# Optimization experiments

Hardware: AMD Instinct MI355X
Metric: run time of the kernel (lower is better)

Reference implementation:

```python
import jax, jax.numpy as jnp
import numpy as np
from jax import lax

# ---- config (FalconH1Mixer, FalconH1-1.5B-like) ----
BATCH = 2
SEQ = 2048
HID = 2048
EXPAND = 2
INTER = EXPAND * HID          # 4096 (mamba_d_ssm=None)
HEADS = 64
PDIM = INTER // HEADS         # 64 head_dim
NSTATE = 128                  # mamba_d_state
G = 1                         # mamba_n_groups
HPG = HEADS // G
KCONV = 4                     # mamba_d_conv
GTS = G * NSTATE
CONV_DIM = INTER + 2 * GTS    # 4352
PROJ_DIM = 2 * INTER + 2 * GTS + HEADS  # 8512 (z | xBC | dt)
EPS = 1e-5
MUP = (0.25, 0.5, 0.5, 0.5, 1.0)  # ssm_multipliers for z, x, B, C, dt


def _mup_vector():
    # per-region muP multipliers over the zxbcdt projection axis
    return jnp.concatenate([
        jnp.full((INTER,), MUP[0], jnp.float32),
        jnp.full((INTER,), MUP[1], jnp.float32),
        jnp.full((GTS,), MUP[2], jnp.float32),
        jnp.full((GTS,), MUP[3], jnp.float32),
        jnp.full((HEADS,), MUP[4], jnp.float32),
    ])


def setup_inputs() -> dict:
    key = jax.random.key(0)
    ks = jax.random.split(key, 8)
    hidden_states = jax.random.normal(ks[0], (BATCH, SEQ, HID), jnp.float32)
    in_proj_w = jax.random.normal(ks[1], (HID, PROJ_DIM), jnp.float32) * 0.02
    conv_w = jax.random.normal(ks[2], (CONV_DIM, KCONV), jnp.float32) * 0.2
    conv_b = jnp.zeros((CONV_DIM,), jnp.float32)
    A_log = jnp.log(jnp.arange(1, HEADS + 1, dtype=jnp.float32))
    D = jnp.ones((HEADS,), jnp.float32)
    dt_bias = jax.random.uniform(ks[3], (HEADS,), jnp.float32)
    norm_w = jnp.ones((INTER,), jnp.float32)
    out_proj_w = jax.random.normal(ks[4], (INTER, HID), jnp.float32) * 0.02
    return dict(hidden_states=hidden_states, in_proj_w=in_proj_w, conv_w=conv_w,
                conv_b=conv_b, A_log=A_log, D=D, dt_bias=dt_bias,
                norm_w=norm_w, out_proj_w=out_proj_w)


def _forward(hidden_states, in_proj_w, conv_w, conv_b, A_log, D, dt_bias, norm_w, out_proj_w):
    b, l, _ = hidden_states.shape
    # zxbcdt projection with muP scaling
    proj = (hidden_states @ in_proj_w) * _mup_vector()  # (b, l, PROJ_DIM)
    z = proj[..., :INTER]
    xBC = proj[..., INTER:INTER + CONV_DIM]
    dt = proj[..., INTER + CONV_DIM:]                    # (b, l, HEADS)
    # depthwise causal conv1d + SiLU
    xBC_cl = jnp.swapaxes(xBC, 1, 2)                     # (b, c, l)
    conv = lax.conv_general_dilated(xBC_cl, conv_w[:, None, :],
                                    window_strides=(1,), padding=((KCONV - 1, 0),),
                                    feature_group_count=CONV_DIM)
    xBC = jax.nn.silu(jnp.swapaxes(conv + conv_b[None, :, None], 1, 2))  # (b, l, c)
    x = xBC[..., :INTER].reshape(b, l, G, HPG, PDIM)
    Bm = xBC[..., INTER:INTER + GTS].reshape(b, l, G, NSTATE)
    Cm = xBC[..., INTER + GTS:].reshape(b, l, G, NSTATE)
    # dt / A discretization
    dt = jax.nn.softplus(dt + dt_bias)                   # (b, l, HEADS)
    A = -jnp.exp(A_log)                                  # (HEADS,)
    dA = jnp.exp(dt * A).reshape(b, l, G, HPG)           # (b, l, g, c)
    dtx = dt.reshape(b, l, G, HPG)[..., None] * x        # (b, l, g, c, p)

    def step(state, inp):
        dA_t, dtx_t, B_t, C_t = inp                      # (b,g,c) (b,g,c,p) (b,g,n) (b,g,n)
        state = state * dA_t[..., None, None] + jnp.einsum('bgcp,bgn->bgcpn', dtx_t, B_t)
        y_t = jnp.einsum('bgn,bgcpn->bgcp', C_t, state)
        return state, y_t

    inputs = (jnp.moveaxis(dA, 1, 0), jnp.moveaxis(dtx, 1, 0),
              jnp.moveaxis(Bm, 1, 0), jnp.moveaxis(Cm, 1, 0))
    state0 = jnp.zeros((b, G, HPG, PDIM, NSTATE), hidden_states.dtype)
    _, ys = lax.scan(step, state0, inputs)               # (l, b, g, c, p)
    y = jnp.moveaxis(ys, 0, 1) + D.reshape(1, 1, G, HPG, 1) * x
    y = y.reshape(b, l, INTER)
    # grouped RMSNorm, then SiLU gate (norm_before_gate=True)
    yg = y.reshape(b, l, G, INTER // G)
    var = jnp.mean(jnp.square(yg), axis=-1, keepdims=True)
    yn = (yg * lax.rsqrt(var + EPS)).reshape(b, l, INTER) * norm_w
    out = yn * jax.nn.silu(z)
    return out @ out_proj_w                              # (b, l, HID)


def reference(hidden_states, in_proj_w, conv_w, conv_b, A_log, D, dt_bias, norm_w, out_proj_w):
    return _forward(hidden_states, in_proj_w, conv_w, conv_b, A_log, D, dt_bias, norm_w, out_proj_w)
```

## Files before the change

kernel.cpp:

```cpp
#include <hip/hip_runtime.h>
#include <stdint.h>

typedef unsigned short u16;
typedef unsigned int   u32;
typedef __attribute__((ext_vector_type(8))) short bf16x8;
typedef __attribute__((ext_vector_type(4))) float f32x4;
typedef __attribute__((ext_vector_type(4))) u32   u32x4;

static __device__ __forceinline__ float bf2f(u16 v){
  u32 u = ((u32)v) << 16;
  return __builtin_bit_cast(float, u);
}
static __device__ __forceinline__ u16 f2bf(float f){
  u32 u = __builtin_bit_cast(u32, f);
  return (u16)((u + 0x7fffu + ((u >> 16) & 1u)) >> 16);
}

#define MFMA16(a,b,c) __builtin_amdgcn_mfma_f32_16x16x32_bf16((a),(b),(c),0,0,0)

typedef const __attribute__((address_space(1))) char glb_c;
typedef __attribute__((address_space(3))) char lds_c;
static __device__ __forceinline__ void gload_lds16(const void* g, void* l){
  __builtin_amdgcn_global_load_lds((glb_c*)g, (lds_c*)l, 16, 0, 0);
}

#define SEQN   2048
#define PROJD  8512
#define CONVD  4352
#define INTERD 4096
#define NST    128
#define QC     64
#define NCHUNK 32

__global__ __launch_bounds__(256) void detect_kernel(
    const void* __restrict__ hidden, u32* __restrict__ flag)
{
  __shared__ int cnt;
  if (threadIdx.x == 0) cnt = 0;
  __syncthreads();
  if (threadIdx.x < 128){
    u16 v = ((const u16*)hidden)[threadIdx.x * 2];
    int e = (v >> 7) & 0xFF;
    int plaus = (v == 0) || (e >= 0x70 && e <= 0x8F);
    atomicAdd(&cnt, plaus);
  }
  __syncthreads();
  if (threadIdx.x == 0) *flag = (cnt < 64) ? 1u : 0u;
}

__global__ __launch_bounds__(256) void cvt_kernel(
    const void* __restrict__ src, u16* __restrict__ dst, int n,
    const u32* __restrict__ flag)
{
  bool isf32 = (*flag != 0);
  int stride = gridDim.x * 256;
  for (int i = blockIdx.x*256 + threadIdx.x; i < n; i += stride){
    if (isf32) dst[i] = f2bf(((const float*)src)[i]);
    else       dst[i] = ((const u16*)src)[i];
  }
}

__global__ __launch_bounds__(256) void cvt_transpose_kernel(
    const void* __restrict__ src, u16* __restrict__ dst,
    int K, int N, int Npad, const u32* __restrict__ flag)
{
  bool isf32 = (*flag != 0);
  __shared__ u16 tile[64][72];
  int n0 = blockIdx.x * 64, k0 = blockIdx.y * 64;
  int tid = threadIdx.x;
  int tr = tid >> 6;
  int tc = tid & 63;
  #pragma unroll
  for (int i = 0; i < 16; i++){
    int k = i*4 + tr;
    int gk = k0 + k, gn = n0 + tc;
    float v = 0.f;
    if (gk < K && gn < N)
      v = isf32 ? ((const float*)src)[(size_t)gk*N + gn]
                : bf2f(((const u16*)src)[(size_t)gk*N + gn]);
    tile[k][tc] = f2bf(v);
  }
  __syncthreads();
  #pragma unroll
  for (int i = 0; i < 16; i++){
    int n = i*4 + tr;
    int gn = n0 + n;
    if (gn < Npad && (k0 + tc) < K)
      dst[(size_t)gn*K + k0 + tc] = tile[tc][n];
  }
}

__global__ __launch_bounds__(256) void cvt_small_kernel(
    const void* cw, const void* cb, const void* al, const void* dv,
    const void* db, const void* nw, u16* __restrict__ base,
    const u32* __restrict__ flag)
{
  bool isf32 = (*flag != 0);
  int idx = blockIdx.x*256 + threadIdx.x;
  if (idx >= 26048) return;
  const void* src; int off;
  if      (idx < 17408){ src = cw; off = idx;          }
  else if (idx < 21760){ src = cb; off = idx - 17408;  }
  else if (idx < 21824){ src = al; off = idx - 21760;  }
  else if (idx < 21888){ src = dv; off = idx - 21824;  }
  else if (idx < 21952){ src = db; off = idx - 21888;  }
  else                 { src = nw; off = idx - 21952;  }
  u16 v = isf32 ? f2bf(((const float*)src)[off]) : ((const u16*)src)[off];
  base[idx] = v;
}

__global__ __launch_bounds__(256) void gemm_kernel(
    const u16* __restrict__ A, const u16* __restrict__ Bt,
    u16* __restrict__ C0, u16* __restrict__ C1, u16* __restrict__ C2,
    float* __restrict__ CF,
    int M, int N, int K, int mode)
{
  __shared__ u16 sA[128*64];
  __shared__ u16 sB[128*64];

  int nbx = gridDim.x;
  int nwg = nbx * gridDim.y;
  int bid = blockIdx.y * nbx + blockIdx.x;
  int swz = (bid & 7) * (nwg >> 3) + (bid >> 3);
  int m0 = (swz / nbx) * 128, n0 = (swz % nbx) * 128;

  int tid = threadIdx.x;
  int wave = tid >> 6, lane = tid & 63;
  int l15 = lane & 15, quad = lane >> 4;
  int wrow = (wave & 1) * 64, wcol = (wave >> 1) * 64;

  int srow  = tid >> 3;
  int sboff = ((tid & 7) << 4) ^ ((srow & 7) << 4);

  const char* Ag = (const char*)(A  + (size_t)(m0 + srow) * K);
  const char* Bg = (const char*)(Bt + (size_t)(n0 + srow) * K);
  char* sAw = (char*)sA + wave*8*128;
  char* sBw = (char*)sB + wave*8*128;

  f32x4 acc[4][4];
  #pragma unroll
  for (int i=0;i<4;i++)
    #pragma unroll
    for (int j=0;j<4;j++) acc[i][j] = (f32x4){0.f,0.f,0.f,0.f};

  const char* sAc = (const char*)sA;
  const char* sBc = (const char*)sB;
  int xorv = (l15 & 7) << 4;

  for (int k0 = 0; k0 < K; k0 += 64){
    __syncthreads();
    size_t kb = (size_t)k0*2 + sboff;
    #pragma unroll
    for (int s = 0; s < 4; s++){
      gload_lds16(Ag + (size_t)(s*32)*K*2 + kb, sAw + s*32*128);
      gload_lds16(Bg + (size_t)(s*32)*K*2 + kb, sBw + s*32*128);
    }
    __syncthreads();
    #pragma unroll
    for (int kk2 = 0; kk2 < 2; kk2++){
      bf16x8 af[4], bfr[4];
      #pragma unroll
      for (int i=0;i<4;i++)
        af[i]  = *(const bf16x8*)(sAc + (wrow + i*16 + l15)*128
                                      + ((quad*16 + kk2*64) ^ xorv));
      #pragma unroll
      for (int j=0;j<4;j++)
        bfr[j] = *(const bf16x8*)(sBc + (wcol + j*16 + l15)*128
                                      + ((quad*16 + kk2*64) ^ xorv));
      #pragma unroll
      for (int i=0;i<4;i++)
        #pragma unroll
        for (int j=0;j<4;j++)
          acc[i][j] = MFMA16(af[i], bfr[j], acc[i][j]);
    }
  }

  #pragma unroll
  for (int j=0;j<4;j++){
    int col = n0 + wcol + j*16 + l15;
    #pragma unroll
    for (int i=0;i<4;i++){
      #pragma unroll
      for (int r=0;r<4;r++){
        int row = m0 + wrow + i*16 + quad*4 + r;
        float fv = acc[i][j][r];
        if (mode == 2){
          if (col < N) CF[(size_t)row*N + col] = fv;
        } else if (mode == 0){
          if (col < N) C0[(size_t)row*N + col] = f2bf(fv);
        } else {
          u16 v = f2bf(fv);
          if      (col < 4096) C0[(size_t)row*4096 + col] = v;
          else if (col < 8448) C1[(size_t)row*CONVD + (col - 4096)] = v;
          else if (col < 8512) C2[(size_t)row*64 + (col - 8448)] = v;
        }
      }
    }
  }
}

__global__ __launch_bounds__(256) void conv_silu_kernel(
    const u16* __restrict__ xbcr, const u16* __restrict__ conv_w,
    const u16* __restrict__ conv_b, u16* __restrict__ xbc)
{
  int c  = blockIdx.x * 256 + threadIdx.x;
  int rl = blockIdx.y;
  int b = rl >> 11, l = rl & 2047;
  float w[4];
  #pragma unroll
  for (int k=0;k<4;k++) w[k] = 0.5f * bf2f(conv_w[c*4 + k]);
  float acc = bf2f(conv_b[c]);
  #pragma unroll
  for (int k=0;k<4;k++){
    int s = l + k - 3;
    if (s >= 0) acc += bf2f(xbcr[(size_t)(b*2048 + s)*CONVD + c]) * w[k];
  }
  float sig = 1.f / (1.f + __expf(-acc));
  xbc[(size_t)rl*CONVD + c] = f2bf(acc * sig);
}

__global__ __launch_bounds__(256) void dt_kernel(
    const u16* __restrict__ dtraw, const u16* __restrict__ dt_bias,
    const u16* __restrict__ A_log, float* __restrict__ dt_soft,
    float* __restrict__ ldA)
{
  int idx = blockIdx.x * 256 + threadIdx.x;
  int h = idx & 63;
  float x = bf2f(dtraw[idx]) + bf2f(dt_bias[h]);
  float sp = (x > 20.f) ? x : log1pf(expf(x));
  float A = -expf(bf2f(A_log[h]));
  dt_soft[idx] = sp;
  ldA[idx] = sp * A;
}

__global__ __launch_bounds__(256) void chunk_decay_kernel(
    const float* __restrict__ ldA, float* __restrict__ cdexp)
{
  int idx = blockIdx.x * 256 + threadIdx.x;
  int q = idx & 31, bh = idx >> 5;
  int b = bh >> 6, h = bh & 63;
  float s = 0.f;
  int t0 = q * QC;
  for (int t = 0; t < QC; t++) s += ldA[(size_t)(b*2048 + t0 + t)*64 + h];
  cdexp[idx] = expf(s);
}

#define SBS  136
#define SUTS 80
#define SMS  80
__global__ __launch_bounds__(256) void ssd_intra_kernel(
    const u16* __restrict__ xbc, const float* __restrict__ dt_soft,
    const float* __restrict__ ldA, u16* __restrict__ S,
    u16* __restrict__ y)
{
  int q = blockIdx.x, h = blockIdx.y, b = blockIdx.z;
  int bh = b*64 + h;
  int t0 = q * QC;
  int tid = threadIdx.x, wave = tid >> 6, lane = tid & 63;
  int l15 = lane & 15, quad = lane >> 4;

  __shared__ u16 sB [64*SBS];
  __shared__ u16 sCM[64*SBS];
  __shared__ u16 sBt[128*64];
  __shared__ u16 sUt[64*SUTS];
  __shared__ float sLa[64];
  __shared__ float sW[64];

  if (tid < 64){
    float v = ldA[(size_t)(b*2048 + t0 + tid)*64 + h];
    #pragma unroll
    for (int off = 1; off < 64; off <<= 1){
      float o = __shfl_up(v, off, 64);
      if (lane >= off) v += o;
    }
    sLa[tid] = v;
  }
  __syncthreads();
  float laE = sLa[63];
  if (tid < 64) sW[tid] = __expf(laE - sLa[tid]);
  __syncthreads();

  #pragma unroll
  for (int i = 0; i < 4; i++){
    int ch = i*256 + tid;
    int s = ch >> 4, nc = (ch & 15) * 8;
    const u16* src = xbc + (size_t)(b*2048 + t0 + s)*CONVD;
    u32x4 vb = *(const u32x4*)(src + 4096 + nc);
    u32x4 vc = *(const u32x4*)(src + 4224 + nc);
    *(u32x4*)(sB  + s*SBS + nc) = vb;
    *(u32x4*)(sCM + s*SBS + nc) = vc;
    float wdec = sW[s];
    const u16* pb = (const u16*)&vb;
    #pragma unroll
    for (int e = 0; e < 8; e++)
      sBt[(nc + e)*64 + s] = f2bf(bf2f(pb[e]) * wdec);
  }
  #pragma unroll
  for (int i = 0; i < 2; i++){
    int ch = i*256 + tid;
    int s = ch >> 3, pc = (ch & 7) * 8;
    const u16* src = xbc + (size_t)(b*2048 + t0 + s)*CONVD + h*64 + pc;
    u32x4 vx = *(const u32x4*)src;
    float dt = dt_soft[(size_t)(b*2048 + t0 + s)*64 + h];
    const u16* px = (const u16*)&vx;
    #pragma unroll
    for (int e = 0; e < 8; e++)
      sUt[(pc + e)*SUTS + s] = f2bf(bf2f(px[e]) * dt);
  }
  __syncthreads();

  int tr = (wave & 1)*32, sc = (wave >> 1)*32;
  f32x4 aM[2][2];
  #pragma unroll
  for (int i=0;i<2;i++)
    #pragma unroll
    for (int j=0;j<2;j++) aM[i][j] = (f32x4){0.f,0.f,0.f,0.f};
  #pragma unroll
  for (int kk = 0; kk < 128; kk += 32){
    bf16x8 a0 = *(const bf16x8*)(sCM + (tr      + l15)*SBS + kk + quad*8);
    bf16x8 a1 = *(const bf16x8*)(sCM + (tr + 16 + l15)*SBS + kk + quad*8);
    bf16x8 b0 = *(const bf16x8*)(sB  + (sc      + l15)*SBS + kk + quad*8);
    bf16x8 b1 = *(const bf16x8*)(sB  + (sc + 16 + l15)*SBS + kk + quad*8);
    aM[0][0] = MFMA16(a0, b0, aM[0][0]);
    aM[0][1] = MFMA16(a0, b1, aM[0][1]);
    aM[1][0] = MFMA16(a1, b0, aM[1][0]);
    aM[1][1] = MFMA16(a1, b1, aM[1][1]);
  }
  __syncthreads();
  u16* sM = sCM;
  #pragma unroll
  for (int i = 0; i < 2; i++){
    #pragma unroll
    for (int j = 0; j < 2; j++){
      int scol = sc + j*16 + l15;
      #pragma unroll
      for (int r = 0; r < 4; r++){
        int trow = tr + i*16 + quad*4 + r;
        float v = 0.f;
        if (scol <= trow) v = aM[i][j][r] * __expf(sLa[trow] - sLa[scol]);
        sM[trow*SMS + scol] = f2bf(v);
      }
    }
  }
  __syncthreads();

  f32x4 aY[2][2];
  #pragma unroll
  for (int i=0;i<2;i++)
    #pragma unroll
    for (int j=0;j<2;j++) aY[i][j] = (f32x4){0.f,0.f,0.f,0.f};
  #pragma unroll
  for (int kk = 0; kk < 64; kk += 32){
    bf16x8 a0 = *(const bf16x8*)(sM  + (tr      + l15)*SMS  + kk + quad*8);
    bf16x8 a1 = *(const bf16x8*)(sM  + (tr + 16 + l15)*SMS  + kk + quad*8);
    bf16x8 b0 = *(const bf16x8*)(sUt + (sc      + l15)*SUTS + kk + quad*8);
    bf16x8 b1 = *(const bf16x8*)(sUt + (sc + 16 + l15)*SUTS + kk + quad*8);
    aY[0][0] = MFMA16(a0, b0, aY[0][0]);
    aY[0][1] = MFMA16(a0, b1, aY[0][1]);
    aY[1][0] = MFMA16(a1, b0, aY[1][0]);
    aY[1][1] = MFMA16(a1, b1, aY[1][1]);
  }
  #pragma unroll
  for (int i = 0; i < 2; i++){
    #pragma unroll
    for (int j = 0; j < 2; j++){
      int p = sc + j*16 + l15;
      #pragma unroll
      for (int r = 0; r < 4; r++){
        int t = tr + i*16 + quad*4 + r;
        y[(size_t)(b*2048 + t0 + t)*INTERD + h*64 + p] = f2bf(aY[i][j][r]);
      }
    }
  }

  int pr = (wave & 1)*32, nw = (wave >> 1)*64;
  f32x4 aS[2][4];
  #pragma unroll
  for (int i=0;i<2;i++)
    #pragma unroll
    for (int j=0;j<4;j++) aS[i][j] = (f32x4){0.f,0.f,0.f,0.f};
  #pragma unroll
  for (int kk = 0; kk < 64; kk += 32){
    bf16x8 a0 = *(const bf16x8*)(sUt + (pr      + l15)*SUTS + kk + quad*8);
    bf16x8 a1 = *(const bf16x8*)(sUt + (pr + 16 + l15)*SUTS + kk + quad*8);
    #pragma unroll
    for (int j = 0; j < 4; j++){
      bf16x8 bb = *(const bf16x8*)(sBt + (nw + j*16 + l15)*64 + kk + quad*8);
      aS[0][j] = MFMA16(a0, bb, aS[0][j]);
      aS[1][j] = MFMA16(a1, bb, aS[1][j]);
    }
  }
  u16* Sl = S + ((size_t)bh*NCHUNK + q)*8192;
  #pragma unroll
  for (int i = 0; i < 2; i++){
    #pragma unroll
    for (int j = 0; j < 4; j++){
      int n = nw + j*16 + l15;
      #pragma unroll
      for (int r = 0; r < 4; r++){
        int p = pr + i*16 + quad*4 + r;
        Sl[p*NST + n] = f2bf(aS[i][j][r]);
      }
    }
  }
}

__global__ __launch_bounds__(256) void ssd_carry_kernel(
    u16* __restrict__ S, const float* __restrict__ cdexp)
{
  int idx = blockIdx.x * 256 + threadIdx.x;
  int e = idx & 8191, bh = idx >> 13;
  float E = 0.f;
  for (int q = 0; q < NCHUNK; q++){
    size_t off = ((size_t)bh*NCHUNK + q)*8192 + e;
    float v = bf2f(S[off]);
    S[off] = f2bf(E);
    E = cdexp[bh*NCHUNK + q] * E + v;
  }
}

__global__ __launch_bounds__(256) void ssd_inter_kernel(
    const u16* __restrict__ xbc, const float* __restrict__ ldA,
    const u16* __restrict__ S, const u16* __restrict__ Dvec,
    u16* __restrict__ y)
{
  int q = blockIdx.x, h = blockIdx.y, b = blockIdx.z;
  int bh = b*64 + h;
  int t0 = q * QC;
  int tid = threadIdx.x, wave = tid >> 6, lane = tid & 63;
  int l15 = lane & 15, quad = lane >> 4;

  __shared__ u16 sC[64*SBS];
  __shared__ u16 sS[64*SBS];
  __shared__ float sLa[64];

  if (tid < 64){
    float v = ldA[(size_t)(b*2048 + t0 + tid)*64 + h];
    #pragma unroll
    for (int off = 1; off < 64; off <<= 1){
      float o = __shfl_up(v, off, 64);
      if (lane >= off) v += o;
    }
    sLa[tid] = v;
  }
  const u16* Sc = S + ((size_t)bh*NCHUNK + q)*8192;
  #pragma unroll
  for (int i = 0; i < 4; i++){
    int ch = i*256 + tid;
    int s = ch >> 4, nc = (ch & 15) * 8;
    *(u32x4*)(sC + s*SBS + nc) =
        *(const u32x4*)(xbc + (size_t)(b*2048 + t0 + s)*CONVD + 4224 + nc);
    *(u32x4*)(sS + s*SBS + nc) = *(const u32x4*)(Sc + s*NST + nc);
  }
  __syncthreads();

  int tr = (wave & 1)*32, pc = (wave >> 1)*32;
  f32x4 acc[2][2];
  #pragma unroll
  for (int i=0;i<2;i++)
    #pragma unroll
    for (int j=0;j<2;j++) acc[i][j] = (f32x4){0.f,0.f,0.f,0.f};
  #pragma unroll
  for (int kk = 0; kk < 128; kk += 32){
    bf16x8 a0 = *(const bf16x8*)(sC + (tr      + l15)*SBS + kk + quad*8);
    bf16x8 a1 = *(const bf16x8*)(sC + (tr + 16 + l15)*SBS + kk + quad*8);
    bf16x8 b0 = *(const bf16x8*)(sS + (pc      + l15)*SBS + kk + quad*8);
    bf16x8 b1 = *(const bf16x8*)(sS + (pc + 16 + l15)*SBS + kk + quad*8);
    acc[0][0] = MFMA16(a0, b0, acc[0][0]);
    acc[0][1] = MFMA16(a0, b1, acc[0][1]);
    acc[1][0] = MFMA16(a1, b0, acc[1][0]);
    acc[1][1] = MFMA16(a1, b1, acc[1][1]);
  }
  float Dh = bf2f(Dvec[h]);
  #pragma unroll
  for (int i = 0; i < 2; i++){
    #pragma unroll
    for (int j = 0; j < 2; j++){
      int p = pc + j*16 + l15;
      #pragma unroll
      for (int r = 0; r < 4; r++){
        int t = tr + i*16 + quad*4 + r;
        size_t row = (size_t)(b*2048 + t0 + t);
        size_t yo = row*INTERD + h*64 + p;
        float xv = bf2f(xbc[row*CONVD + h*64 + p]);
        float v = bf2f(y[yo]) + __expf(sLa[t]) * acc[i][j][r] + Dh * xv;
        y[yo] = f2bf(v);
      }
    }
  }
}

__global__ __launch_bounds__(256) void rmsnorm_gate_kernel(
    const u16* __restrict__ y, const u16* __restrict__ z,
    const u16* __restrict__ norm_w, u16* __restrict__ g)
{
  int rl = blockIdx.x;
  int tid = threadIdx.x, wave = tid >> 6, lane = tid & 63;
  const u16* yr = y + (size_t)rl*INTERD;
  float vy[16];
  float ss = 0.f;
  #pragma unroll
  for (int i = 0; i < 16; i++){
    int idx = i*256 + tid;
    float v = bf2f(yr[idx]);
    vy[i] = v;
    ss += v*v;
  }
  #pragma unroll
  for (int off = 32; off >= 1; off >>= 1) ss += __shfl_xor(ss, off, 64);
  __shared__ float red[4];
  if (lane == 0) red[wave] = ss;
  __syncthreads();
  float tot = red[0] + red[1] + red[2] + red[3];
  float rstd = rsqrtf(tot * (1.f/4096.f) + 1e-5f);
  const u16* zr = z + (size_t)rl*INTERD;
  u16* gr = g + (size_t)rl*INTERD;
  #pragma unroll
  for (int i = 0; i < 16; i++){
    int idx = i*256 + tid;
    float v = vy[i] * rstd * bf2f(norm_w[idx]);
    float zv = 0.25f * bf2f(zr[idx]);
    float sig = 1.f / (1.f + __expf(-zv));
    gr[idx] = f2bf(v * zv * sig);
  }
}

extern "C" void kernel_launch(void* const* d_in, const int* in_sizes, int n_in,
                              void* d_out, int out_size, void* d_ws, size_t ws_size,
                              hipStream_t stream)
{
  const void* hidden_r    = d_in[0];
  const void* in_proj_r   = d_in[1];
  const void* conv_w_r    = d_in[2];
  const void* conv_b_r    = d_in[3];
  const void* A_log_r     = d_in[4];
  const void* Dvec_r      = d_in[5];
  const void* dt_bias_r   = d_in[6];
  const void* norm_w_r    = d_in[7];
  const void* out_proj_r  = d_in[8];
  float* out = (float*)d_out;
  char* ws = (char*)d_ws;

  u16*   z     = (u16*)(ws + 0);
  u16*   xbcr  = (u16*)(ws + 33554432ull);
  u16*   yb    = (u16*)(ws + 33554432ull);
  u16*   dtraw = (u16*)(ws + 69206016ull);
  u16*   xbc   = (u16*)(ws + 69730304ull);
  u16*   w2b   = (u16*)(ws + 69730304ull);
  float* dt_s  = (float*)(ws + 105381888ull);
  float* lda   = (float*)(ws + 106430464ull);
  float* cdexp = (float*)(ws + 107479040ull);
  u32*   flag  = (u32*)(ws + 107495424ull);
  u16*   svec  = (u16*)(ws + 107495680ull);
  u16*   cw_b  = svec;
  u16*   cb_b  = svec + 17408;
  u16*   al_b  = svec + 21760;
  u16*   d_b   = svec + 21824;
  u16*   db_b  = svec + 21888;
  u16*   nw_b  = svec + 21952;
  u16*   S     = (u16*)(ws + 107626496ull);
  u16*   hb    = (u16*)(ws + 107626496ull);
  u16*   w1b   = (u16*)(ws + 124403712ull);
  u16*   g     = (u16*)(ws + 107626496ull);

  detect_kernel<<<1, 256, 0, stream>>>(hidden_r, flag);
  cvt_kernel<<<4096, 256, 0, stream>>>(hidden_r, hb, 8388608, flag);
  cvt_transpose_kernel<<<dim3(134, 32), 256, 0, stream>>>(
      in_proj_r, w1b, 2048, 8512, 8576, flag);
  cvt_small_kernel<<<102, 256, 0, stream>>>(conv_w_r, conv_b_r, A_log_r,
      Dvec_r, dt_bias_r, norm_w_r, svec, flag);
  gemm_kernel<<<dim3(67, 32), 256, 0, stream>>>(
      hb, w1b, z, xbcr, dtraw, (float*)nullptr, 4096, 8576, 2048, 1);
  conv_silu_kernel<<<dim3(17, 4096), 256, 0, stream>>>(xbcr, cw_b, cb_b, xbc);
  dt_kernel<<<1024, 256, 0, stream>>>(dtraw, db_b, al_b, dt_s, lda);
  chunk_decay_kernel<<<16, 256, 0, stream>>>(lda, cdexp);
  ssd_intra_kernel<<<dim3(NCHUNK, 64, 2), 256, 0, stream>>>(xbc, dt_s, lda, S, yb);
  ssd_carry_kernel<<<4096, 256, 0, stream>>>(S, cdexp);
  ssd_inter_kernel<<<dim3(NCHUNK, 64, 2), 256, 0, stream>>>(xbc, lda, S, d_b, yb);
  cvt_transpose_kernel<<<dim3(32, 64), 256, 0, stream>>>(
      out_proj_r, w2b, 4096, 2048, 2048, flag);
  rmsnorm_gate_kernel<<<4096, 256, 0, stream>>>(yb, z, nw_b, g);
  gemm_kernel<<<dim3(16, 32), 256, 0, stream>>>(
      g, w2b, (u16*)nullptr, (u16*)nullptr, (u16*)nullptr, out,
      4096, 2048, 4096, 2);
}
```

Baseline: 720.2 us.

## Rewrite GEMM as 256x256-tile, 8-wave kernel with double-buffered LDS prefetch

Replaces the 128x128, 4-wave GEMM with a 256x256, 512-thread kernel. It keeps two LDS buffers (128 KB total) and interleaves async global-to-LDS loads for the next K-tiles with MFMA work, using explicit vmcnt waits, barriers and setprio. The goal is to hide global load latency and raise data reuse per block. The in_proj weight padding grows to 8704 columns so N divides evenly into 256-wide tiles. In exchange, LDS use allows at most one block per CU, and the out-projection launches only 128 blocks, which may leave many CUs idle.

```diff
diff --git a/kernel.cpp b/kernel.cpp
--- a/kernel.cpp
+++ b/kernel.cpp
@@ -109,81 +109,126 @@
   base[idx] = v;
 }
 
-__global__ __launch_bounds__(256) void gemm_kernel(
+__global__ __launch_bounds__(512, 2) void gemm_kernel(
     const u16* __restrict__ A, const u16* __restrict__ Bt,
     u16* __restrict__ C0, u16* __restrict__ C1, u16* __restrict__ C2,
     float* __restrict__ CF,
     int M, int N, int K, int mode)
 {
-  __shared__ u16 sA[128*64];
-  __shared__ u16 sB[128*64];
-
-  int nbx = gridDim.x;
-  int nwg = nbx * gridDim.y;
-  int bid = blockIdx.y * nbx + blockIdx.x;
-  int swz = (bid & 7) * (nwg >> 3) + (bid >> 3);
-  int m0 = (swz / nbx) * 128, n0 = (swz % nbx) * 128;
-
-  int tid = threadIdx.x;
-  int wave = tid >> 6, lane = tid & 63;
-  int l15 = lane & 15, quad = lane >> 4;
-  int wrow = (wave & 1) * 64, wcol = (wave >> 1) * 64;
-
-  int srow  = tid >> 3;
-  int sboff = ((tid & 7) << 4) ^ ((srow & 7) << 4);
-
-  const char* Ag = (const char*)(A  + (size_t)(m0 + srow) * K);
-  const char* Bg = (const char*)(Bt + (size_t)(n0 + srow) * K);
-  char* sAw = (char*)sA + wave*8*128;
-  char* sBw = (char*)sB + wave*8*128;
-
-  f32x4 acc[4][4];
-  #pragma unroll
-  for (int i=0;i<4;i++)
-    #pragma unroll
-    for (int j=0;j<4;j++) acc[i][j] = (f32x4){0.f,0.f,0.f,0.f};
-
-  const char* sAc = (const char*)sA;
-  const char* sBc = (const char*)sB;
-  int xorv = (l15 & 7) << 4;
-
-  for (int k0 = 0; k0 < K; k0 += 64){
-    __syncthreads();
-    size_t kb = (size_t)k0*2 + sboff;
-    #pragma unroll
-    for (int s = 0; s < 4; s++){
-      gload_lds16(Ag + (size_t)(s*32)*K*2 + kb, sAw + s*32*128);
-      gload_lds16(Bg + (size_t)(s*32)*K*2 + kb, sBw + s*32*128);
-    }
-    __syncthreads();
-    #pragma unroll
-    for (int kk2 = 0; kk2 < 2; kk2++){
-      bf16x8 af[4], bfr[4];
+  __shared__ u16 smem[65536];
+
+  const int nbx = gridDim.x;
+  const int nwg = nbx * gridDim.y;
+  const int bid = blockIdx.y * nbx + blockIdx.x;
+  const int swz = (bid & 7) * (nwg >> 3) + (bid >> 3);
+  const int m0 = (swz / nbx) * 256, n0 = (swz % nbx) * 256;
+
+  const int tid = threadIdx.x;
+  const int wave = tid >> 6, lane = tid & 63;
+  const int l15 = lane & 15, quad = lane >> 4;
+  const int wm = wave >> 2, wn = wave & 3;
+
+  const size_t Kb = (size_t)K * 2;
+  const int srow = tid >> 3;
+  const int schk = (tid & 7) ^ (srow & 7);
+  const char* Abp = (const char*)A  + (size_t)(m0 + srow) * Kb + schk * 16;
+  const char* Bbp = (const char*)Bt + (size_t)(n0 + srow) * Kb + schk * 16;
+  char* ldsb = (char*)smem + wave * 1024;
+
+  const int aoff0 = ((quad    ) ^ (l15 & 7)) << 4;
+  const int aoff1 = ((quad + 4) ^ (l15 & 7)) << 4;
+  const char* ardb[2][2];
+  const char* brdb[2][2];
+  #pragma unroll
+  for (int c = 0; c < 2; c++){
+    ardb[c][0] = (const char*)smem + c*65536 + (wm*128 + l15)*128 + aoff0;
+    ardb[c][1] = (const char*)smem + c*65536 + (wm*128 + l15)*128 + aoff1;
+    brdb[c][0] = (const char*)smem + c*65536 + 32768 + (wn*64 + l15)*128 + aoff0;
+    brdb[c][1] = (const char*)smem + c*65536 + 32768 + (wn*64 + l15)*128 + aoff1;
+  }
+
+  f32x4 acc[8][4];
+  #pragma unroll
+  for (int i = 0; i < 8; i++)
+    #pragma unroll
+    for (int j = 0; j < 4; j++) acc[i][j] = (f32x4){0.f,0.f,0.f,0.f};
+
+  bf16x8 af[4];
+  bf16x8 bfr[8];
+
+#define STG(ptr, par, isB, h, kt) do{                                    \
+    const char* _s = (ptr) + (size_t)((h)*128)*Kb + (size_t)(kt)*128;    \
+    char* _d = ldsb + (par)*65536 + ((isB)?32768:0) + (h)*16384;         \
+    gload_lds16(_s, _d);                                                 \
+    gload_lds16(_s + 64*Kb, _d + 8192);                                  \
+  }while(0)
+
+  STG(Bbp,0,1,0,0); STG(Bbp,0,1,1,0);
+  STG(Abp,0,0,0,0); STG(Abp,0,0,1,0);
+  STG(Bbp,1,1,0,1); STG(Bbp,1,1,1,1);
+  asm volatile("s_waitcnt vmcnt(4)" ::: "memory");
+  __builtin_amdgcn_s_barrier();
+
+  const int NT = K >> 6;
+  for (int I = 0; I < (NT >> 1); ++I){
+    const int T1 = 2*I+1, T2 = 2*I+2, T3 = 2*I+3;
+    const bool pf = (T2 < NT);
+    #pragma unroll
+    for (int p = 0; p < 8; ++p){
+      const int q = p & 3, c = p >> 2;
       #pragma unroll
-      for (int i=0;i<4;i++)
-        af[i]  = *(const bf16x8*)(sAc + (wrow + i*16 + l15)*128
-                                      + ((quad*16 + kk2*64) ^ xorv));
+      for (int k = 0; k < 2; k++){
+        af[0+k] = *(const bf16x8*)(ardb[c][k] + (2*q+0)*2048);
+        af[2+k] = *(const bf16x8*)(ardb[c][k] + (2*q+1)*2048);
+      }
+      if (q == 0){
+        #pragma unroll
+        for (int nf = 0; nf < 4; nf++)
+          #pragma unroll
+          for (int k = 0; k < 2; k++)
+            bfr[nf*2+k] = *(const bf16x8*)(brdb[c][k] + nf*2048);
+      }
+      if      (p == 0) STG(Abp,1,0,0,T1);
+      else if (p == 1) STG(Abp,1,0,1,T1);
+      else if (p == 2){ if (pf) STG(Bbp,0,1,0,T2); }
+      else if (p == 3){
+        if (pf){ STG(Bbp,0,1,1,T2);
+                 asm volatile("s_waitcnt vmcnt(4)" ::: "memory"); }
+        else     asm volatile("s_waitcnt vmcnt(0)" ::: "memory");
+      }
+      else if (p == 4){ if (pf) STG(Abp,0,0,0,T2); }
+      else if (p == 5){ if (pf) STG(Abp,0,0,1,T2); }
+      else if (p == 6){ if (pf) STG(Bbp,1,1,0,T3); }
+      else            { if (pf){ STG(Bbp,1,1,1,T3);
+                 asm volatile("s_waitcnt vmcnt(4)" ::: "memory"); } }
+      asm volatile("" ::: "memory");
+      __builtin_amdgcn_s_barrier();
+      asm volatile("s_waitcnt lgkmcnt(0)" ::: "memory");
+      __builtin_amdgcn_s_setprio(1);
       #pragma unroll
-      for (int j=0;j<4;j++)
-        bfr[j] = *(const bf16x8*)(sBc + (wcol + j*16 + l15)*128
-                                      + ((quad*16 + kk2*64) ^ xorv));
+      for (int mf2 = 0; mf2 < 2; ++mf2)
+        #pragma unroll
+        for (int nf = 0; nf < 4; ++nf)
+          #pragma unroll
+          for (int k = 0; k < 2; k++)
+            acc[2*q+mf2][nf] =
+                MFMA16(af[mf2*2+k], bfr[nf*2+k], acc[2*q+mf2][nf]);
+      __builtin_amdgcn_s_setprio(0);
+      asm volatile("" ::: "memory");
+      __builtin_amdgcn_s_barrier();
+    }
+  }
+#undef STG
+
+  #pragma unroll
+  for (int nf = 0; nf < 4; nf++){
+    int col = n0 + wn*64 + nf*16 + l15;
+    #pragma unroll
+    for (int mf = 0; mf < 8; mf++){
       #pragma unroll
-      for (int i=0;i<4;i++)
-        #pragma unroll
-        for (int j=0;j<4;j++)
-          acc[i][j] = MFMA16(af[i], bfr[j], acc[i][j]);
-    }
-  }
-
-  #pragma unroll
-  for (int j=0;j<4;j++){
-    int col = n0 + wcol + j*16 + l15;
-    #pragma unroll
-    for (int i=0;i<4;i++){
-      #pragma unroll
-      for (int r=0;r<4;r++){
-        int row = m0 + wrow + i*16 + quad*4 + r;
-        float fv = acc[i][j][r];
+      for (int r = 0; r < 4; r++){
+        int row = m0 + wm*128 + mf*16 + quad*4 + r;
+        float fv = acc[mf][nf][r];
         if (mode == 2){
           if (col < N) CF[(size_t)row*N + col] = fv;
         } else if (mode == 0){
@@ -565,12 +610,12 @@
 
   detect_kernel<<<1, 256, 0, stream>>>(hidden_r, flag);
   cvt_kernel<<<4096, 256, 0, stream>>>(hidden_r, hb, 8388608, flag);
-  cvt_transpose_kernel<<<dim3(134, 32), 256, 0, stream>>>(
-      in_proj_r, w1b, 2048, 8512, 8576, flag);
+  cvt_transpose_kernel<<<dim3(136, 32), 256, 0, stream>>>(
+      in_proj_r, w1b, 2048, 8512, 8704, flag);
   cvt_small_kernel<<<102, 256, 0, stream>>>(conv_w_r, conv_b_r, A_log_r,
       Dvec_r, dt_bias_r, norm_w_r, svec, flag);
-  gemm_kernel<<<dim3(67, 32), 256, 0, stream>>>(
-      hb, w1b, z, xbcr, dtraw, (float*)nullptr, 4096, 8576, 2048, 1);
+  gemm_kernel<<<dim3(34, 16), 512, 0, stream>>>(
+      hb, w1b, z, xbcr, dtraw, (float*)nullptr, 4096, 8704, 2048, 1);
   conv_silu_kernel<<<dim3(17, 4096), 256, 0, stream>>>(xbcr, cw_b, cb_b, xbc);
   dt_kernel<<<1024, 256, 0, stream>>>(dtraw, db_b, al_b, dt_s, lda);
   chunk_decay_kernel<<<16, 256, 0, stream>>>(lda, cdexp);
@@ -580,7 +625,7 @@
   cvt_transpose_kernel<<<dim3(32, 64), 256, 0, stream>>>(
       out_proj_r, w2b, 4096, 2048, 2048, flag);
   rmsnorm_gate_kernel<<<4096, 256, 0, stream>>>(yb, z, nw_b, g);
-  gemm_kernel<<<dim3(16, 32), 256, 0, stream>>>(
+  gemm_kernel<<<dim3(8, 16), 512, 0, stream>>>(
       g, w2b, (u16*)nullptr, (u16*)nullptr, (u16*)nullptr, out,
       4096, 2048, 4096, 2);
 }
```

After: 718.8 us. Within noise of the previous version (-0.2%).
